# Kernel optimization log

Hardware: AMD Instinct MI355X
Metric: run time of the kernel (lower is better)

## Reference

```python
import jax, jax.numpy as jnp
import numpy as np
from jax import lax

N, D1, D2, H, W = 1, 32, 32, 128, 160


def l1_normalize(k, eps=1e-12):
    # F.normalize(k, p=1, dim=1): divide by max(sum |k|, eps) over channel dim
    denom = jnp.maximum(jnp.sum(jnp.abs(k), axis=1, keepdims=True), eps)
    return k / denom


def _scan_forward(x, k):
    """Recurrent SGA-style scan along axis 2 (forward).
    x: (N, C, S, T) cost slices; k: (N, 5, S, T) normalized guidance.
    out(s) = k0*x(s) + k1*out(s-1) + k2*out_{c-1}(s-1) + k3*out_{c+1}(s-1)
             + k4*max_c out(s-1);  out(0) = x(0) at the boundary.
    """
    xs = jnp.moveaxis(x, 2, 0)   # (S, N, C, T)
    ks = jnp.moveaxis(k, 2, 0)   # (S, N, 5, T)
    init = xs[0]                 # (N, C, T)

    def step(prev, inp):
        xr, kr = inp
        k0, k1, k2, k3, k4 = jnp.split(kr, 5, axis=1)            # each (N,1,T)
        pm1 = jnp.concatenate([jnp.zeros_like(prev[:, :1]), prev[:, :-1]], axis=1)
        pp1 = jnp.concatenate([prev[:, 1:], jnp.zeros_like(prev[:, :1])], axis=1)
        pmx = jnp.max(prev, axis=1, keepdims=True)
        out = k0 * xr + k1 * prev + k2 * pm1 + k3 * pp1 + k4 * pmx
        return out, out

    _, rest = lax.scan(step, init, (xs[1:], ks[1:]))
    out = jnp.concatenate([init[None], rest], axis=0)
    return jnp.moveaxis(out, 0, 2)


def nlf_dir(x, k, axis, reverse):
    """One directional aggregation pass. axis in {2 (H), 3 (W)}."""
    if reverse:
        x = jnp.flip(x, axis); k = jnp.flip(k, axis)
    if axis == 3:
        x = x.swapaxes(2, 3); k = k.swapaxes(2, 3)
    out = _scan_forward(x, k)
    if axis == 3:
        out = out.swapaxes(2, 3)
    if reverse:
        out = jnp.flip(out, axis)
    return out


def nlf_forward(x, g):
    n, d1, d2, h, w = x.shape
    xc = x.reshape(n, d1 * d2, h, w)
    k1, k2, k3, k4 = jnp.split(g, 4, axis=1)
    k1 = l1_normalize(k1); k2 = l1_normalize(k2)
    k3 = l1_normalize(k3); k4 = l1_normalize(k4)
    xc = nlf_dir(xc, k1, axis=2, reverse=False)   # down
    xc = nlf_dir(xc, k2, axis=2, reverse=True)    # up
    xc = nlf_dir(xc, k3, axis=3, reverse=False)   # right
    xc = nlf_dir(xc, k4, axis=3, reverse=True)    # left
    return xc.reshape(n, d1, d2, h, w)


def setup_inputs() -> dict:
    key = jax.random.key(0)
    kx, kg = jax.random.split(key)
    x = jax.random.normal(kx, (N, D1, D2, H, W), dtype=jnp.float32)
    g = jax.random.normal(kg, (N, 20, H, W), dtype=jnp.float32)
    return {"x": x, "g": g}


def reference(x, g):
    return nlf_forward(x, g)
```

## Files before the change

### kernel.cpp

```cpp
#include <hip/hip_runtime.h>

#define Hh 128
#define Ww 160
#define Cc 1024
#define HWp (Hh*Ww)

template<int CTRL>
__device__ __forceinline__ float dppMaxStage(float v) {
    int t = __builtin_amdgcn_update_dpp((int)0xFF800000, __float_as_int(v),
                                        CTRL, 0xF, 0xF, false);
    return fmaxf(v, __int_as_float(t));
}
__device__ __forceinline__ float waveMaxDpp(float v) {
    v = dppMaxStage<0x111>(v);
    v = dppMaxStage<0x112>(v);
    v = dppMaxStage<0x114>(v);
    v = dppMaxStage<0x118>(v);
    v = dppMaxStage<0x142>(v);
    v = dppMaxStage<0x143>(v);
    return __int_as_float(__builtin_amdgcn_readlane(__float_as_int(v), 63));
}
__device__ __forceinline__ float dppRor1(float v) {
    return __int_as_float(__builtin_amdgcn_update_dpp(0, __float_as_int(v),
                                                      0x13C, 0xF, 0xF, false));
}
__device__ __forceinline__ float dppRol1(float v) {
    return __int_as_float(__builtin_amdgcn_update_dpp(0, __float_as_int(v),
                                                      0x134, 0xF, 0xF, false));
}

__global__ __launch_bounds__(256) void norm_g(const float* __restrict__ g,
                                              float* __restrict__ kn)
{
    int p = blockIdx.x * blockDim.x + threadIdx.x;
    if (p >= HWp) return;
    int s = p / Ww, t = p - s * Ww;
    #pragma unroll
    for (int d = 0; d < 4; ++d) {
        float v[5]; float sum = 0.f;
        #pragma unroll
        for (int j = 0; j < 5; ++j) {
            v[j] = g[(size_t)(5 * d + j) * HWp + p];
            sum += fabsf(v[j]);
        }
        float inv = 1.f / fmaxf(sum, 1e-12f);
        size_t off = (d < 2) ? ((size_t)d * HWp * 5 + ((size_t)t * Hh + s) * 5)
                             : ((size_t)d * HWp * 5 + (size_t)p * 5);
        #pragma unroll
        for (int j = 0; j < 5; ++j) kn[off + j] = v[j] * inv;
    }
}

__global__ __launch_bounds__(256) void transpose_in(const float* __restrict__ in,
                                                    float* __restrict__ out)
{
    __shared__ float tile[32][33];
    int p0 = blockIdx.x * 32, c0 = blockIdx.y * 32;
    int tx = threadIdx.x, ty = threadIdx.y;
    #pragma unroll
    for (int i = 0; i < 4; ++i)
        tile[ty + 8 * i][tx] = in[(size_t)(c0 + ty + 8 * i) * HWp + p0 + tx];
    __syncthreads();
    #pragma unroll
    for (int i = 0; i < 4; ++i)
        out[(size_t)(p0 + ty + 8 * i) * Cc + c0 + tx] = tile[tx][ty + 8 * i];
}

__global__ __launch_bounds__(256) void transpose_out(const float* __restrict__ Y,
                                                     float* __restrict__ out)
{
    __shared__ float tile[32][33];
    int c0 = blockIdx.x * 32, p0 = blockIdx.y * 32;
    int tx = threadIdx.x, ty = threadIdx.y;
    #pragma unroll
    for (int i = 0; i < 4; ++i)
        tile[ty + 8 * i][tx] = Y[(size_t)(p0 + ty + 8 * i) * Cc + c0 + tx];
    __syncthreads();
    #pragma unroll
    for (int i = 0; i < 4; ++i)
        out[(size_t)(c0 + ty + 8 * i) * HWp + p0 + tx] = tile[tx][ty + 8 * i];
}

template<int NSTEPS, long STRIDE, long COLSTRIDE, bool FWD>
__global__ __launch_bounds__(64) void scan_pass(float* __restrict__ Y,
                                                const float* __restrict__ ktab)
{
    __shared__ float ks_raw[Ww * 5 + 16];
    float* ks = ks_raw + 8;
    const int l = threadIdx.x;

    const float* kt = ktab + (size_t)blockIdx.x * (size_t)(NSTEPS * 5);
    for (int i = l; i < NSTEPS * 5; i += 64) ks[i] = kt[i];
    __syncthreads();

    constexpr long SSTEP = FWD ? STRIDE : -STRIDE;
    constexpr int  KSTEP = FWD ? 1 : -1;
    long cur = (long)blockIdx.x * COLSTRIDE + (FWD ? 0L : (long)(NSTEPS - 1) * STRIDE);
    int kidx = FWD ? 0 : NSTEPS - 1;
    const int loff = 4 * l;

    float4 prev[4];
    #pragma unroll
    for (int q = 0; q < 4; ++q)
        prev[q] = *reinterpret_cast<const float4*>(&Y[cur + q * 256 + loff]);
    float mx = -3.4e38f;
    #pragma unroll
    for (int q = 0; q < 4; ++q)
        mx = fmaxf(mx, fmaxf(fmaxf(prev[q].x, prev[q].y),
                             fmaxf(prev[q].z, prev[q].w)));
    float pmax = waveMaxDpp(mx);

    float4 xb0[4], xb1[4], xb2[4];
    #pragma unroll
    for (int q = 0; q < 4; ++q)
        xb0[q] = *reinterpret_cast<const float4*>(&Y[cur + SSTEP + q * 256 + loff]);
    #pragma unroll
    for (int q = 0; q < 4; ++q)
        xb1[q] = *reinterpret_cast<const float4*>(&Y[cur + 2 * SSTEP + q * 256 + loff]);
    #pragma unroll
    for (int q = 0; q < 4; ++q)
        xb2[q] = *reinterpret_cast<const float4*>(&Y[cur + 3 * SSTEP + q * 256 + loff]);

    kidx += KSTEP;
    float pk0 = ks[kidx * 5 + 0], pk1 = ks[kidx * 5 + 1], pk2 = ks[kidx * 5 + 2],
          pk3 = ks[kidx * 5 + 3], pk4 = ks[kidx * 5 + 4];

    cur += SSTEP;
    int i = 1;

#define STEP(XB)                                                              \
  {                                                                           \
    const float k0 = pk0, k1 = pk1, k2 = pk2, k3 = pk3, k4 = pk4;             \
    kidx += KSTEP;                                                            \
    pk0 = ks[kidx * 5 + 0]; pk1 = ks[kidx * 5 + 1]; pk2 = ks[kidx * 5 + 2];   \
    pk3 = ks[kidx * 5 + 3]; pk4 = ks[kidx * 5 + 4];                           \
    float A[4], B[4];                                                         \
    _Pragma("unroll") for (int q = 0; q < 4; ++q) {                           \
      A[q] = dppRor1(prev[q].w);               \
      B[q] = dppRol1(prev[q].x);               \
    }                                                                         \
    float4 pt[4]; float m = -3.4e38f;                                         \
    _Pragma("unroll") for (int q = 0; q < 4; ++q) {                           \
      float pm0 = (l > 0)  ? A[q] : (q > 0 ? A[q - 1] : 0.f);                 \
      float pp3 = (l < 63) ? B[q] : (q < 3 ? B[q + 1] : 0.f);                 \
      float4 p = prev[q], x = XB[q];                                          \
      pt[q].x = k0 * x.x + k1 * p.x + k2 * pm0 + k3 * p.y;                    \
      pt[q].y = k0 * x.y + k1 * p.y + k2 * p.x + k3 * p.z;                    \
      pt[q].z = k0 * x.z + k1 * p.z + k2 * p.y + k3 * p.w;                    \
      pt[q].w = k0 * x.w + k1 * p.w + k2 * p.z + k3 * pp3;                    \
      m = fmaxf(m, fmaxf(fmaxf(pt[q].x, pt[q].y), fmaxf(pt[q].z, pt[q].w)));  \
    }                                                                         \
    if (i + 3 < NSTEPS) {                                                     \
      _Pragma("unroll") for (int q = 0; q < 4; ++q)                           \
        XB[q] = *reinterpret_cast<const float4*>(                             \
            &Y[cur + 3 * SSTEP + q * 256 + loff]);                            \
    }                                                                         \
    float R = waveMaxDpp(m);                                                  \
    _Pragma("unroll") for (int q = 0; q < 4; ++q) {                           \
      prev[q].x = fmaf(k4, pmax, pt[q].x);                                    \
      prev[q].y = fmaf(k4, pmax, pt[q].y);                                    \
      prev[q].z = fmaf(k4, pmax, pt[q].z);                                    \
      prev[q].w = fmaf(k4, pmax, pt[q].w);                                    \
      *reinterpret_cast<float4*>(&Y[cur + q * 256 + loff]) = prev[q];         \
    }                                                                         \
    pmax = fmaf(k4, pmax, R);                                                 \
    cur += SSTEP; ++i;                                                        \
  }

    while (i + 2 < NSTEPS) { STEP(xb0) STEP(xb1) STEP(xb2) }
    if (i < NSTEPS) STEP(xb0)
    if (i < NSTEPS) STEP(xb1)
#undef STEP
}

extern "C" void kernel_launch(void* const* d_in, const int* in_sizes, int n_in,
                              void* d_out, int out_size, void* d_ws, size_t ws_size,
                              hipStream_t stream)
{
    const float* x = (const float*)d_in[0];
    const float* g = (const float*)d_in[1];
    float* out = (float*)d_out;

    const size_t kn_bytes = (size_t)4 * HWp * 5 * sizeof(float);
    const size_t y_bytes  = (size_t)Cc * HWp * sizeof(float);
    if (ws_size < kn_bytes + y_bytes) return;

    float* kn = (float*)d_ws;
    float* Y  = (float*)((char*)d_ws + kn_bytes);

    norm_g<<<(HWp + 255) / 256, 256, 0, stream>>>(g, kn);

    transpose_in<<<dim3(HWp / 32, Cc / 32), dim3(32, 8), 0, stream>>>(x, Y);

    scan_pass<Hh, (long)Ww * Cc, (long)Cc, true ><<<Ww, 64, 0, stream>>>(
        Y, kn + (size_t)0 * HWp * 5);
    scan_pass<Hh, (long)Ww * Cc, (long)Cc, false><<<Ww, 64, 0, stream>>>(
        Y, kn + (size_t)1 * HWp * 5);
    scan_pass<Ww, (long)Cc, (long)Ww * Cc, true ><<<Hh, 64, 0, stream>>>(
        Y, kn + (size_t)2 * HWp * 5);
    scan_pass<Ww, (long)Cc, (long)Ww * Cc, false><<<Hh, 64, 0, stream>>>(
        Y, kn + (size_t)3 * HWp * 5);

    transpose_out<<<dim3(Cc / 32, HWp / 32), dim3(32, 8), 0, stream>>>(Y, out);
}
```

Before: 288.5 us.

## Split scan channels across four waves with LDS halo and max exchange

Each scan block now uses 256 threads (four waves) instead of one wave, and each thread holds one float4 of channels rather than four. Channel-neighbour halos and per-wave maxima are exchanged through double-buffered shared memory, with a barrier on every step. The global max term is folded in lazily: the current step's max is computed before the k4*pmax offset is added, and the offset is carried forward. This spreads the serial per-step work over more waves to raise parallelism and latency hiding, at the cost of a block-wide barrier per scan step.

```diff
diff --git a/kernel.cpp b/kernel.cpp
--- a/kernel.cpp
+++ b/kernel.cpp
@@ -82,94 +82,89 @@
 }
 
 template<int NSTEPS, long STRIDE, long COLSTRIDE, bool FWD>
-__global__ __launch_bounds__(64) void scan_pass(float* __restrict__ Y,
-                                                const float* __restrict__ ktab)
+__global__ __launch_bounds__(256) void scan_pass(float* __restrict__ Y,
+                                                 const float* __restrict__ ktab)
 {
     __shared__ float ks_raw[Ww * 5 + 16];
+    __shared__ float xch[2][4][4];
     float* ks = ks_raw + 8;
-    const int l = threadIdx.x;
+    const int tid = threadIdx.x;
+    const int l = tid & 63;
+    const int w = tid >> 6;
 
     const float* kt = ktab + (size_t)blockIdx.x * (size_t)(NSTEPS * 5);
-    for (int i = l; i < NSTEPS * 5; i += 64) ks[i] = kt[i];
-    __syncthreads();
+    for (int i = tid; i < NSTEPS * 5; i += 256) ks[i] = kt[i];
 
     constexpr long SSTEP = FWD ? STRIDE : -STRIDE;
     constexpr int  KSTEP = FWD ? 1 : -1;
     long cur = (long)blockIdx.x * COLSTRIDE + (FWD ? 0L : (long)(NSTEPS - 1) * STRIDE);
     int kidx = FWD ? 0 : NSTEPS - 1;
-    const int loff = 4 * l;
-
-    float4 prev[4];
-    #pragma unroll
-    for (int q = 0; q < 4; ++q)
-        prev[q] = *reinterpret_cast<const float4*>(&Y[cur + q * 256 + loff]);
-    float mx = -3.4e38f;
-    #pragma unroll
-    for (int q = 0; q < 4; ++q)
-        mx = fmaxf(mx, fmaxf(fmaxf(prev[q].x, prev[q].y),
-                             fmaxf(prev[q].z, prev[q].w)));
-    float pmax = waveMaxDpp(mx);
-
-    float4 xb0[4], xb1[4], xb2[4];
-    #pragma unroll
-    for (int q = 0; q < 4; ++q)
-        xb0[q] = *reinterpret_cast<const float4*>(&Y[cur + SSTEP + q * 256 + loff]);
-    #pragma unroll
-    for (int q = 0; q < 4; ++q)
-        xb1[q] = *reinterpret_cast<const float4*>(&Y[cur + 2 * SSTEP + q * 256 + loff]);
-    #pragma unroll
-    for (int q = 0; q < 4; ++q)
-        xb2[q] = *reinterpret_cast<const float4*>(&Y[cur + 3 * SSTEP + q * 256 + loff]);
+    const int off4 = 4 * tid;
+
+    float4 prev = *reinterpret_cast<const float4*>(&Y[cur + off4]);
+    float4 xb0 = *reinterpret_cast<const float4*>(&Y[cur + 1 * SSTEP + off4]);
+    float4 xb1 = *reinterpret_cast<const float4*>(&Y[cur + 2 * SSTEP + off4]);
+    float4 xb2 = *reinterpret_cast<const float4*>(&Y[cur + 3 * SSTEP + off4]);
+    float4 xb3 = *reinterpret_cast<const float4*>(&Y[cur + 4 * SSTEP + off4]);
+
+    float m0 = fmaxf(fmaxf(prev.x, prev.y), fmaxf(prev.z, prev.w));
+    float R0 = waveMaxDpp(m0);
+    __syncthreads();
+    if (l == 0)  { xch[0][w][0] = prev.x; xch[0][w][2] = R0; }
+    if (l == 63) { xch[0][w][1] = prev.w; }
+    float a_prev = 0.f;
 
     kidx += KSTEP;
     float pk0 = ks[kidx * 5 + 0], pk1 = ks[kidx * 5 + 1], pk2 = ks[kidx * 5 + 2],
           pk3 = ks[kidx * 5 + 3], pk4 = ks[kidx * 5 + 4];
 
+    asm volatile("s_waitcnt lgkmcnt(0)\n\ts_barrier" ::: "memory");
     cur += SSTEP;
     int i = 1;
 
-#define STEP(XB)                                                              \
+#define STEP(XB, RP, WP)                                                      \
   {                                                                           \
     const float k0 = pk0, k1 = pk1, k2 = pk2, k3 = pk3, k4 = pk4;             \
     kidx += KSTEP;                                                            \
     pk0 = ks[kidx * 5 + 0]; pk1 = ks[kidx * 5 + 1]; pk2 = ks[kidx * 5 + 2];   \
     pk3 = ks[kidx * 5 + 3]; pk4 = ks[kidx * 5 + 4];                           \
-    float A[4], B[4];                                                         \
-    _Pragma("unroll") for (int q = 0; q < 4; ++q) {                           \
-      A[q] = dppRor1(prev[q].w);               \
-      B[q] = dppRol1(prev[q].x);               \
-    }                                                                         \
-    float4 pt[4]; float m = -3.4e38f;                                         \
-    _Pragma("unroll") for (int q = 0; q < 4; ++q) {                           \
-      float pm0 = (l > 0)  ? A[q] : (q > 0 ? A[q - 1] : 0.f);                 \
-      float pp3 = (l < 63) ? B[q] : (q < 3 ? B[q + 1] : 0.f);                 \
-      float4 p = prev[q], x = XB[q];                                          \
-      pt[q].x = k0 * x.x + k1 * p.x + k2 * pm0 + k3 * p.y;                    \
-      pt[q].y = k0 * x.y + k1 * p.y + k2 * p.x + k3 * p.z;                    \
-      pt[q].z = k0 * x.z + k1 * p.z + k2 * p.y + k3 * p.w;                    \
-      pt[q].w = k0 * x.w + k1 * p.w + k2 * p.z + k3 * pp3;                    \
-      m = fmaxf(m, fmaxf(fmaxf(pt[q].x, pt[q].y), fmaxf(pt[q].z, pt[q].w)));  \
-    }                                                                         \
-    if (i + 3 < NSTEPS) {                                                     \
-      _Pragma("unroll") for (int q = 0; q < 4; ++q)                           \
-        XB[q] = *reinterpret_cast<const float4*>(                             \
-            &Y[cur + 3 * SSTEP + q * 256 + loff]);                            \
-    }                                                                         \
-    float R = waveMaxDpp(m);                                                  \
-    _Pragma("unroll") for (int q = 0; q < 4; ++q) {                           \
-      prev[q].x = fmaf(k4, pmax, pt[q].x);                                    \
-      prev[q].y = fmaf(k4, pmax, pt[q].y);                                    \
-      prev[q].z = fmaf(k4, pmax, pt[q].z);                                    \
-      prev[q].w = fmaf(k4, pmax, pt[q].w);                                    \
-      *reinterpret_cast<float4*>(&Y[cur + q * 256 + loff]) = prev[q];         \
-    }                                                                         \
-    pmax = fmaf(k4, pmax, R);                                                 \
+                                                  \
+    float nbrLo = (w > 0) ? xch[RP][w - 1][1] : 0.f;                          \
+    float nbrHi = (w < 3) ? xch[RP][w + 1][0] : 0.f;                          \
+    float Rg = fmaxf(fmaxf(xch[RP][0][2], xch[RP][1][2]),                     \
+                     fmaxf(xch[RP][2][2], xch[RP][3][2]));                    \
+    float Mp = Rg + a_prev;                           \
+    float a  = k4 * Mp;                                                       \
+    float A = dppRor1(prev.w);                 \
+    float B = dppRol1(prev.x);                 \
+    float pm0 = (l > 0)  ? A : nbrLo;                                         \
+    float pp3 = (l < 63) ? B : nbrHi;                                         \
+    float4 pt;                                                                \
+    pt.x = k0 * XB.x + k1 * prev.x + k2 * pm0    + k3 * prev.y;               \
+    pt.y = k0 * XB.y + k1 * prev.y + k2 * prev.x + k3 * prev.z;               \
+    pt.z = k0 * XB.z + k1 * prev.z + k2 * prev.y + k3 * prev.w;               \
+    pt.w = k0 * XB.w + k1 * prev.w + k2 * prev.z + k3 * pp3;                  \
+    float4 o;                                                                 \
+    o.x = pt.x + a; o.y = pt.y + a; o.z = pt.z + a; o.w = pt.w + a;           \
+    *reinterpret_cast<float4*>(&Y[cur + off4]) = o;                           \
+    float m = fmaxf(fmaxf(pt.x, pt.y), fmaxf(pt.z, pt.w));                    \
+    float Rw = waveMaxDpp(m);                                                 \
+    if (l == 0)  { xch[WP][w][0] = o.x; xch[WP][w][2] = Rw; }                 \
+    if (l == 63) { xch[WP][w][1] = o.w; }                                     \
+    if (i + 4 < NSTEPS)                                                       \
+      XB = *reinterpret_cast<const float4*>(&Y[cur + 4 * SSTEP + off4]);      \
+    a_prev = a;                                                               \
+    asm volatile("s_waitcnt lgkmcnt(0)\n\ts_barrier" ::: "memory");           \
+    prev = o;                                                                 \
     cur += SSTEP; ++i;                                                        \
   }
 
-    while (i + 2 < NSTEPS) { STEP(xb0) STEP(xb1) STEP(xb2) }
-    if (i < NSTEPS) STEP(xb0)
-    if (i < NSTEPS) STEP(xb1)
+    while (i + 3 < NSTEPS) {
+        STEP(xb0, 0, 1) STEP(xb1, 1, 0) STEP(xb2, 0, 1) STEP(xb3, 1, 0)
+    }
+    if (i < NSTEPS) STEP(xb0, 0, 1)
+    if (i < NSTEPS) STEP(xb1, 1, 0)
+    if (i < NSTEPS) STEP(xb2, 0, 1)
 #undef STEP
 }
 
@@ -192,13 +187,13 @@
 
     transpose_in<<<dim3(HWp / 32, Cc / 32), dim3(32, 8), 0, stream>>>(x, Y);
 
-    scan_pass<Hh, (long)Ww * Cc, (long)Cc, true ><<<Ww, 64, 0, stream>>>(
+    scan_pass<Hh, (long)Ww * Cc, (long)Cc, true ><<<Ww, 256, 0, stream>>>(
         Y, kn + (size_t)0 * HWp * 5);
-    scan_pass<Hh, (long)Ww * Cc, (long)Cc, false><<<Ww, 64, 0, stream>>>(
+    scan_pass<Hh, (long)Ww * Cc, (long)Cc, false><<<Ww, 256, 0, stream>>>(
         Y, kn + (size_t)1 * HWp * 5);
-    scan_pass<Ww, (long)Cc, (long)Ww * Cc, true ><<<Hh, 64, 0, stream>>>(
+    scan_pass<Ww, (long)Cc, (long)Ww * Cc, true ><<<Hh, 256, 0, stream>>>(
         Y, kn + (size_t)2 * HWp * 5);
-    scan_pass<Ww, (long)Cc, (long)Ww * Cc, false><<<Hh, 64, 0, stream>>>(
+    scan_pass<Ww, (long)Cc, (long)Ww * Cc, false><<<Hh, 256, 0, stream>>>(
         Y, kn + (size_t)3 * HWp * 5);
 
     transpose_out<<<dim3(Cc / 32, HWp / 32), dim3(32, 8), 0, stream>>>(Y, out);
```

New measurement: 241.8 us. 1.19x faster.
